# Kernel tuning notes

Measured on AMD Instinct MI355X. Metric: run time of the kernel, lower is better.

## Reference

```python
import jax, jax.numpy as jnp
import numpy as np

QMAX = 127.0          # int8 clip bound (symmetric, preserve-zero)
QDIV = 127.5          # AQT int8 scale divisor: 2**(bits-1) - 0.5


def _safe(s):
    # avoid div-by-zero for all-zero rows/cols
    return jnp.where(s == 0.0, 1.0, s)


def setup_inputs() -> dict:
    key = jax.random.key(0)
    k1, k2 = jax.random.split(key)
    lhs = jax.random.normal(k1, (8192, 4096), dtype=jnp.float32)
    rhs = jax.random.normal(k2, (4096, 4096), dtype=jnp.float32)
    return {"lhs": lhs, "rhs": rhs}


def reference(lhs, rhs):
    # --- dynamic symmetric int8 quantization (AQT abs-max calibration) ---
    # lhs: contract over axis 1 -> per-row scale [M, 1]
    s_l = _safe(jnp.max(jnp.abs(lhs), axis=1, keepdims=True) / QDIV)
    # rhs: contract over axis 0 -> per-column scale [1, N]
    s_r = _safe(jnp.max(jnp.abs(rhs), axis=0, keepdims=True) / QDIV)

    q_l = jnp.clip(jnp.round(lhs / s_l), -QMAX, QMAX).astype(jnp.int8)
    q_r = jnp.clip(jnp.round(rhs / s_r), -QMAX, QMAX).astype(jnp.int8)

    # --- integer matmul with int32 accumulation ---
    acc = jax.lax.dot_general(
        q_l, q_r,
        dimension_numbers=(((1,), (0,)), ((), ())),
        preferred_element_type=jnp.int32,
    )

    # --- dequantize: outer product of per-row / per-column scales ---
    return acc.astype(jnp.float32) * s_l * s_r
```

## Files before the change

kernel.cpp:

```cpp
#include <hip/hip_runtime.h>
#include <stdint.h>

#define M_DIM 8192
#define N_DIM 4096
#define K_DIM 4096
#define QMAXF 127.0f
#define QDIVF 127.5f

typedef int v4i __attribute__((ext_vector_type(4)));

typedef __attribute__((address_space(3))) void lds_void_t;
typedef __attribute__((address_space(1))) const void glb_void_t;

static __device__ __forceinline__ void load_lds16(const void* g, void* l) {
    __builtin_amdgcn_global_load_lds((glb_void_t*)g, (lds_void_t*)l, 16, 0, 0);
}

__global__ __launch_bounds__(256) void row_scale_kernel(
        const float* __restrict__ lhs, float* __restrict__ sL) {
    const int row = blockIdx.x;
    const float4* rp = (const float4*)(lhs + (size_t)row * K_DIM);
    const int t = threadIdx.x;
    float m = 0.0f;
#pragma unroll
    for (int i = 0; i < 4; ++i) {
        float4 v = rp[t + i * 256];
        m = fmaxf(m, fmaxf(fmaxf(fabsf(v.x), fabsf(v.y)),
                           fmaxf(fabsf(v.z), fabsf(v.w))));
    }
#pragma unroll
    for (int off = 32; off; off >>= 1) m = fmaxf(m, __shfl_down(m, off, 64));
    __shared__ float wmax[4];
    if ((t & 63) == 0) wmax[t >> 6] = m;
    __syncthreads();
    if (t == 0) {
        float mm = fmaxf(fmaxf(wmax[0], wmax[1]), fmaxf(wmax[2], wmax[3]));
        float s = mm / QDIVF;
        sL[row] = (s == 0.0f) ? 1.0f : s;
    }
}

__global__ __launch_bounds__(256) void col_absmax_kernel(
        const float* __restrict__ rhs, unsigned* __restrict__ bits) {
    const int col = blockIdx.x * 256 + threadIdx.x;
    const int r0 = blockIdx.y * 64;
    float m = 0.0f;
#pragma unroll 4
    for (int r = 0; r < 64; ++r)
        m = fmaxf(m, fabsf(rhs[(size_t)(r0 + r) * N_DIM + col]));
    atomicMax(&bits[col], __float_as_uint(m));
}

__global__ __launch_bounds__(256) void col_scale_kernel(
        const unsigned* __restrict__ bits, float* __restrict__ sR) {
    const int c = blockIdx.x * 256 + threadIdx.x;
    float s = __uint_as_float(bits[c]) / QDIVF;
    sR[c] = (s == 0.0f) ? 1.0f : s;
}

__global__ __launch_bounds__(256) void quant_lhs_kernel(
        const float* __restrict__ lhs, const float* __restrict__ sL,
        int8_t* __restrict__ ql) {
    const size_t idx = (size_t)blockIdx.x * 256 + threadIdx.x;
    const int row = (int)(idx >> 10);
    const float s = sL[row];
    float4 v = ((const float4*)lhs)[idx];
    int q0 = (int)fminf(fmaxf(rintf(v.x / s), -QMAXF), QMAXF);
    int q1 = (int)fminf(fmaxf(rintf(v.y / s), -QMAXF), QMAXF);
    int q2 = (int)fminf(fmaxf(rintf(v.z / s), -QMAXF), QMAXF);
    int q3 = (int)fminf(fmaxf(rintf(v.w / s), -QMAXF), QMAXF);
    unsigned packed = (q0 & 255) | ((q1 & 255) << 8) | ((q2 & 255) << 16)
                    | ((unsigned)(q3 & 255) << 24);
    ((unsigned*)ql)[idx] = packed;
}

__global__ __launch_bounds__(256) void quant_rhs_t_kernel(
        const float* __restrict__ rhs, const float* __restrict__ sR,
        int8_t* __restrict__ qbT) {
    __shared__ __align__(16) int8_t lt[64][80];
    const int n0 = blockIdx.x * 64;
    const int k0 = blockIdx.y * 64;
    const int t = threadIdx.x;
    const int nloc = t & 63;
    const int kq = (t >> 6) * 16;
    const float s = sR[n0 + nloc];
#pragma unroll
    for (int i = 0; i < 4; ++i) {
        unsigned pack = 0;
#pragma unroll
        for (int j = 0; j < 4; ++j) {
            int kk = kq + i * 4 + j;
            float x = rhs[(size_t)(k0 + kk) * N_DIM + n0 + nloc];
            int q = (int)fminf(fmaxf(rintf(x / s), -QMAXF), QMAXF);
            pack |= (unsigned)(q & 255) << (8 * j);
        }
        *(unsigned*)&lt[nloc][kq + i * 4] = pack;
    }
    __syncthreads();
    const int nn = t >> 2, ch = t & 3;
    v4i val = *(const v4i*)&lt[nn][ch * 16];
    *(v4i*)&qbT[(size_t)(n0 + nn) * K_DIM + k0 + ch * 16] = val;
}

__global__ __launch_bounds__(256, 2) void gemm_i8_kernel(
        const int8_t* __restrict__ qa, const int8_t* __restrict__ qbT,
        const float* __restrict__ sL, const float* __restrict__ sR,
        float* __restrict__ out) {
    __shared__ __align__(16) int8_t lds_a[128 * 64];
    __shared__ __align__(16) int8_t lds_b[128 * 64];

    const int t = threadIdx.x;
    const int wave = t >> 6;
    const int lane = t & 63;
    const int brow = blockIdx.y * 128;
    const int bcol = blockIdx.x * 128;
    const int wm = (wave >> 1) * 64;
    const int wn = (wave & 1) * 64;

    const int srow = t >> 2;
    const int pc = t & 3;
    const int cswz = pc ^ ((srow >> 1) & 3);

    int a_off[4], b_off[4];
#pragma unroll
    for (int m = 0; m < 4; ++m) {
        int row = wm + m * 16 + (lane & 15);
        int pch = (lane >> 4) ^ ((row >> 1) & 3);
        a_off[m] = row * 64 + pch * 16;
    }
#pragma unroll
    for (int n = 0; n < 4; ++n) {
        int row = wn + n * 16 + (lane & 15);
        int pch = (lane >> 4) ^ ((row >> 1) & 3);
        b_off[n] = row * 64 + pch * 16;
    }

    v4i acc[4][4];
#pragma unroll
    for (int m = 0; m < 4; ++m)
#pragma unroll
        for (int n = 0; n < 4; ++n) acc[m][n] = (v4i){0, 0, 0, 0};

    const int8_t* gA = qa  + (size_t)(brow + srow) * K_DIM + cswz * 16;
    const int8_t* gB = qbT + (size_t)(bcol + srow) * K_DIM + cswz * 16;
    const size_t pass_stride = (size_t)64 * K_DIM;

    int8_t* ldsA0 = lds_a + wave * 1024;
    int8_t* ldsA1 = lds_a + 4096 + wave * 1024;
    int8_t* ldsB0 = lds_b + wave * 1024;
    int8_t* ldsB1 = lds_b + 4096 + wave * 1024;

    for (int k0 = 0; k0 < K_DIM; k0 += 64) {
        __syncthreads();
        load_lds16(gA + k0,               ldsA0);
        load_lds16(gA + k0 + pass_stride, ldsA1);
        load_lds16(gB + k0,               ldsB0);
        load_lds16(gB + k0 + pass_stride, ldsB1);
        __syncthreads();

        v4i af[4], bf[4];
#pragma unroll
        for (int m = 0; m < 4; ++m) af[m] = *(const v4i*)(lds_a + a_off[m]);
#pragma unroll
        for (int n = 0; n < 4; ++n) bf[n] = *(const v4i*)(lds_b + b_off[n]);
#pragma unroll
        for (int m = 0; m < 4; ++m)
#pragma unroll
            for (int n = 0; n < 4; ++n)
                acc[m][n] = __builtin_amdgcn_mfma_i32_16x16x64_i8(
                        af[m], bf[n], acc[m][n], 0, 0, 0);
    }

    const int r4 = (lane >> 4) * 4;
    const int cc = lane & 15;
#pragma unroll
    for (int m = 0; m < 4; ++m) {
        const int grow0 = brow + wm + m * 16 + r4;
        const float s0 = sL[grow0 + 0];
        const float s1 = sL[grow0 + 1];
        const float s2 = sL[grow0 + 2];
        const float s3 = sL[grow0 + 3];
#pragma unroll
        for (int n = 0; n < 4; ++n) {
            const int gcol = bcol + wn + n * 16 + cc;
            const float sc = sR[gcol];
            float* o = out + (size_t)grow0 * N_DIM + gcol;
            o[0 * N_DIM] = (float)acc[m][n][0] * s0 * sc;
            o[1 * N_DIM] = (float)acc[m][n][1] * s1 * sc;
            o[2 * N_DIM] = (float)acc[m][n][2] * s2 * sc;
            o[3 * N_DIM] = (float)acc[m][n][3] * s3 * sc;
        }
    }
}

extern "C" void kernel_launch(void* const* d_in, const int* in_sizes, int n_in,
                              void* d_out, int out_size, void* d_ws, size_t ws_size,
                              hipStream_t stream) {
    const float* lhs = (const float*)d_in[0];
    const float* rhs = (const float*)d_in[1];
    float* out = (float*)d_out;

    uint8_t* ws = (uint8_t*)d_ws;
    int8_t* ql    = (int8_t*)ws;
    int8_t* qbT   = (int8_t*)(ws + 33554432);
    float* sL     = (float*)(ws + 50331648);
    float* sR     = (float*)(ws + 50331648 + 32768);
    unsigned* bits = (unsigned*)(ws + 50331648 + 32768 + 16384);

    hipMemsetAsync(bits, 0, N_DIM * sizeof(unsigned), stream);

    row_scale_kernel<<<M_DIM, 256, 0, stream>>>(lhs, sL);
    col_absmax_kernel<<<dim3(N_DIM / 256, K_DIM / 64), 256, 0, stream>>>(rhs, bits);
    col_scale_kernel<<<N_DIM / 256, 256, 0, stream>>>(bits, sR);
    quant_lhs_kernel<<<(M_DIM * K_DIM / 4) / 256, 256, 0, stream>>>(lhs, sL, ql);
    quant_rhs_t_kernel<<<dim3(N_DIM / 64, K_DIM / 64), 256, 0, stream>>>(rhs, sR, qbT);
    gemm_i8_kernel<<<dim3(N_DIM / 128, M_DIM / 128), 256, 0, stream>>>(ql, qbT, sL, sR, out);
}
```

Before: 257.1 us.

## Rewrite int8 GEMM with 256x256 tiles, double-buffered LDS pipeline and block swizzle

Replaces the 128x128, single-stage int8 GEMM with a 512-thread, 256x256-tile kernel using K=128 steps. Global-to-LDS loads for the next tile are interleaved with MFMA phases in a ping-pong buffer, using explicit vmcnt waits, barriers and s_setprio. An XOR LDS swizzle avoids bank conflicts, and the block index is remapped for L2 locality. This targets load latency and synchronisation stalls and increases data reuse. In exchange it uses 128KB of LDS, a large accumulator register footprint, and hand-tuned wait counts that are fragile.

```diff
diff --git a/kernel.cpp b/kernel.cpp
--- a/kernel.cpp
+++ b/kernel.cpp
@@ -102,79 +102,139 @@
     *(v4i*)&qbT[(size_t)(n0 + nn) * K_DIM + k0 + ch * 16] = val;
 }
 
-__global__ __launch_bounds__(256, 2) void gemm_i8_kernel(
+
+#define BAR() do { asm volatile("" ::: "memory");          \
+                   __builtin_amdgcn_s_barrier();           \
+                   asm volatile("" ::: "memory"); } while (0)
+
+#define STAGE_A(h, kt, p) do {                                                        \
+    load_lds16(gA0 + (size_t)((h) * 128) * K_DIM + (size_t)(kt) * 128,                \
+               lds + (p) * 32768 + (h) * 16384 + wb);                                 \
+    load_lds16(gA0 + (size_t)((h) * 128 + 64) * K_DIM + (size_t)(kt) * 128,           \
+               lds + (p) * 32768 + (h) * 16384 + 8192 + wb);                          \
+} while (0)
+
+#define STAGE_B(h, kt, p) do {                                                        \
+    load_lds16(gB0 + (size_t)((h) * 128) * K_DIM + (size_t)(kt) * 128,                \
+               lds + 65536 + (p) * 32768 + (h) * 16384 + wb);                         \
+    load_lds16(gB0 + (size_t)((h) * 128 + 64) * K_DIM + (size_t)(kt) * 128,           \
+               lds + 65536 + (p) * 32768 + (h) * 16384 + 8192 + wb);                  \
+} while (0)
+
+#define MFMA16(MB)                                                                    \
+    _Pragma("unroll") for (int mm = 0; mm < 4; ++mm)                                  \
+    _Pragma("unroll") for (int nn = 0; nn < 4; ++nn)                                  \
+        acc[(MB) + mm][nn] = __builtin_amdgcn_mfma_i32_16x16x64_i8(                   \
+            af[mm], bf[nn], acc[(MB) + mm][nn], 0, 0, 0);
+
+#define TILE(TT, P, S1, S2) do {                                                      \
+                                   \
+    _Pragma("unroll") for (int nn = 0; nn < 4; ++nn)                                  \
+        bf[nn] = *(const v4i*)(lds + (P) * 32768 + boff[nn * 2 + 0]);                 \
+    _Pragma("unroll") for (int mm = 0; mm < 4; ++mm)                                  \
+        af[mm] = *(const v4i*)(lds + (P) * 32768 + aoff[mm * 2 + 0]);                 \
+    if (S1) STAGE_B(1, (TT) + 1, (P) ^ 1);                                            \
+    BAR();                                                                            \
+    __builtin_amdgcn_s_setprio(1); MFMA16(0); __builtin_amdgcn_s_setprio(0);          \
+    BAR();                                                                            \
+                                   \
+    _Pragma("unroll") for (int mm = 0; mm < 4; ++mm)                                  \
+        af[mm] = *(const v4i*)(lds + (P) * 32768 + aoff[(4 + mm) * 2 + 0]);           \
+    if (S1) STAGE_A(0, (TT) + 1, (P) ^ 1);                                            \
+    BAR();                                                                            \
+    __builtin_amdgcn_s_setprio(1); MFMA16(4); __builtin_amdgcn_s_setprio(0);          \
+    BAR();                                                                            \
+                                   \
+    _Pragma("unroll") for (int nn = 0; nn < 4; ++nn)                                  \
+        bf[nn] = *(const v4i*)(lds + (P) * 32768 + boff[nn * 2 + 1]);                 \
+    _Pragma("unroll") for (int mm = 0; mm < 4; ++mm)                                  \
+        af[mm] = *(const v4i*)(lds + (P) * 32768 + aoff[mm * 2 + 1]);                 \
+    if (S1) STAGE_A(1, (TT) + 1, (P) ^ 1);                                            \
+    BAR();                                                                            \
+    __builtin_amdgcn_s_setprio(1); MFMA16(0); __builtin_amdgcn_s_setprio(0);          \
+    BAR();                                                                            \
+                    \
+    _Pragma("unroll") for (int mm = 0; mm < 4; ++mm)                                  \
+        af[mm] = *(const v4i*)(lds + (P) * 32768 + aoff[(4 + mm) * 2 + 1]);           \
+    if (S2) {                                                                         \
+        STAGE_B(0, (TT) + 2, (P));                                                    \
+        asm volatile("s_waitcnt vmcnt(2)" ::: "memory");                              \
+    } else {                                                                          \
+        asm volatile("s_waitcnt vmcnt(0)" ::: "memory");                              \
+    }                                                                                 \
+    BAR();                                                                            \
+    __builtin_amdgcn_s_setprio(1); MFMA16(4); __builtin_amdgcn_s_setprio(0);          \
+    BAR();                                                                            \
+} while (0)
+
+__global__ __launch_bounds__(512, 2) void gemm_i8_kernel(
         const int8_t* __restrict__ qa, const int8_t* __restrict__ qbT,
         const float* __restrict__ sL, const float* __restrict__ sR,
         float* __restrict__ out) {
-    __shared__ __align__(16) int8_t lds_a[128 * 64];
-    __shared__ __align__(16) int8_t lds_b[128 * 64];
+    __shared__ __align__(16) int8_t lds[131072];
 
     const int t = threadIdx.x;
     const int wave = t >> 6;
     const int lane = t & 63;
-    const int brow = blockIdx.y * 128;
-    const int bcol = blockIdx.x * 128;
-    const int wm = (wave >> 1) * 64;
-    const int wn = (wave & 1) * 64;
-
-    const int srow = t >> 2;
-    const int pc = t & 3;
-    const int cswz = pc ^ ((srow >> 1) & 3);
-
-    int a_off[4], b_off[4];
-#pragma unroll
-    for (int m = 0; m < 4; ++m) {
+
+    const int bid = blockIdx.x;
+    const int swz = (bid & 7) * 64 + (bid >> 3);
+    const int brow = (swz & 31) * 256;
+    const int bcol = (swz >> 5) * 256;
+
+    const int wm = (wave >> 2) * 128;
+    const int wn = (wave & 3) * 64;
+
+    int aoff[16];
+    int boff[8];
+#pragma unroll
+    for (int m = 0; m < 8; ++m) {
         int row = wm + m * 16 + (lane & 15);
-        int pch = (lane >> 4) ^ ((row >> 1) & 3);
-        a_off[m] = row * 64 + pch * 16;
+#pragma unroll
+        for (int ks = 0; ks < 2; ++ks)
+            aoff[m * 2 + ks] = row * 128 + ((ks * 4 + (lane >> 4)) ^ (row & 7)) * 16;
     }
 #pragma unroll
     for (int n = 0; n < 4; ++n) {
         int row = wn + n * 16 + (lane & 15);
-        int pch = (lane >> 4) ^ ((row >> 1) & 3);
-        b_off[n] = row * 64 + pch * 16;
-    }
-
-    v4i acc[4][4];
-#pragma unroll
-    for (int m = 0; m < 4; ++m)
+#pragma unroll
+        for (int ks = 0; ks < 2; ++ks)
+            boff[n * 2 + ks] = 65536 + row * 128 + ((ks * 4 + (lane >> 4)) ^ (row & 7)) * 16;
+    }
+
+    v4i acc[8][4];
+#pragma unroll
+    for (int m = 0; m < 8; ++m)
 #pragma unroll
         for (int n = 0; n < 4; ++n) acc[m][n] = (v4i){0, 0, 0, 0};
 
-    const int8_t* gA = qa  + (size_t)(brow + srow) * K_DIM + cswz * 16;
-    const int8_t* gB = qbT + (size_t)(bcol + srow) * K_DIM + cswz * 16;
-    const size_t pass_stride = (size_t)64 * K_DIM;
-
-    int8_t* ldsA0 = lds_a + wave * 1024;
-    int8_t* ldsA1 = lds_a + 4096 + wave * 1024;
-    int8_t* ldsB0 = lds_b + wave * 1024;
-    int8_t* ldsB1 = lds_b + 4096 + wave * 1024;
-
-    for (int k0 = 0; k0 < K_DIM; k0 += 64) {
-        __syncthreads();
-        load_lds16(gA + k0,               ldsA0);
-        load_lds16(gA + k0 + pass_stride, ldsA1);
-        load_lds16(gB + k0,               ldsB0);
-        load_lds16(gB + k0 + pass_stride, ldsB1);
-        __syncthreads();
-
-        v4i af[4], bf[4];
-#pragma unroll
-        for (int m = 0; m < 4; ++m) af[m] = *(const v4i*)(lds_a + a_off[m]);
-#pragma unroll
-        for (int n = 0; n < 4; ++n) bf[n] = *(const v4i*)(lds_b + b_off[n]);
-#pragma unroll
-        for (int m = 0; m < 4; ++m)
-#pragma unroll
-            for (int n = 0; n < 4; ++n)
-                acc[m][n] = __builtin_amdgcn_mfma_i32_16x16x64_i8(
-                        af[m], bf[n], acc[m][n], 0, 0, 0);
-    }
+    const int srow = t >> 3;
+    const int scol = ((t & 7) ^ (srow & 7)) * 16;
+    const int8_t* gA0 = qa  + (size_t)(brow + srow) * K_DIM + scol;
+    const int8_t* gB0 = qbT + (size_t)(bcol + srow) * K_DIM + scol;
+    const int wb = (t >> 6) * 1024;
+
+    v4i af[4], bf[4];
+
+    STAGE_B(0, 0, 0);
+    STAGE_B(1, 0, 0);
+    STAGE_A(0, 0, 0);
+    STAGE_A(1, 0, 0);
+    STAGE_B(0, 1, 1);
+    asm volatile("s_waitcnt vmcnt(2)" ::: "memory");
+    BAR();
+
+    for (int tt = 0; tt < 30; tt += 2) {
+        TILE(tt, 0, 1, 1);
+        TILE(tt + 1, 1, 1, 1);
+    }
+    TILE(30, 0, 1, 0);
+    TILE(31, 1, 0, 0);
 
     const int r4 = (lane >> 4) * 4;
     const int cc = lane & 15;
 #pragma unroll
-    for (int m = 0; m < 4; ++m) {
+    for (int m = 0; m < 8; ++m) {
         const int grow0 = brow + wm + m * 16 + r4;
         const float s0 = sL[grow0 + 0];
         const float s1 = sL[grow0 + 1];
@@ -214,5 +274,5 @@
     col_scale_kernel<<<N_DIM / 256, 256, 0, stream>>>(bits, sR);
     quant_lhs_kernel<<<(M_DIM * K_DIM / 4) / 256, 256, 0, stream>>>(lhs, sL, ql);
     quant_rhs_t_kernel<<<dim3(N_DIM / 64, K_DIM / 64), 256, 0, stream>>>(rhs, sR, qbT);
-    gemm_i8_kernel<<<dim3(N_DIM / 128, M_DIM / 128), 256, 0, stream>>>(ql, qbT, sL, sR, out);
-}
+    gemm_i8_kernel<<<dim3(M_DIM / 256 * N_DIM / 256), 512, 0, stream>>>(ql, qbT, sL, sR, out);
+}
```

Measured after the change: 231.3 us. -10.0%, faster.

## Fuse lhs scale with quantization and rewrite int8 GEMM with 256x256 multistage pipeline

Applied to the files above, without the earlier changes.

Merges the per-row absmax and lhs quantization into one kernel that keeps the row in registers, so lhs is read from memory once instead of twice. The int8 GEMM moves to 256x256 block tiles with 8 waves and a 4-buffer LDS ring filled by direct global-to-LDS loads three tiles ahead. It uses split barriers, explicit vmcnt waits, raised MFMA priority and a swizzled block order for L2 reuse. This adds register pressure and 128KB of LDS per block, which limits occupancy to one block per CU.

```diff
diff --git a/kernel.cpp b/kernel.cpp
--- a/kernel.cpp
+++ b/kernel.cpp
@@ -16,27 +16,38 @@
     __builtin_amdgcn_global_load_lds((glb_void_t*)g, (lds_void_t*)l, 16, 0, 0);
 }
 
-__global__ __launch_bounds__(256) void row_scale_kernel(
-        const float* __restrict__ lhs, float* __restrict__ sL) {
+__global__ __launch_bounds__(256) void row_quant_kernel(
+        const float* __restrict__ lhs, float* __restrict__ sL,
+        int8_t* __restrict__ ql) {
     const int row = blockIdx.x;
     const float4* rp = (const float4*)(lhs + (size_t)row * K_DIM);
     const int t = threadIdx.x;
+    float4 v[4];
     float m = 0.0f;
 #pragma unroll
     for (int i = 0; i < 4; ++i) {
-        float4 v = rp[t + i * 256];
-        m = fmaxf(m, fmaxf(fmaxf(fabsf(v.x), fabsf(v.y)),
-                           fmaxf(fabsf(v.z), fabsf(v.w))));
+        v[i] = rp[t + i * 256];
+        m = fmaxf(m, fmaxf(fmaxf(fabsf(v[i].x), fabsf(v[i].y)),
+                           fmaxf(fabsf(v[i].z), fabsf(v[i].w))));
     }
 #pragma unroll
     for (int off = 32; off; off >>= 1) m = fmaxf(m, __shfl_down(m, off, 64));
     __shared__ float wmax[4];
     if ((t & 63) == 0) wmax[t >> 6] = m;
     __syncthreads();
-    if (t == 0) {
-        float mm = fmaxf(fmaxf(wmax[0], wmax[1]), fmaxf(wmax[2], wmax[3]));
-        float s = mm / QDIVF;
-        sL[row] = (s == 0.0f) ? 1.0f : s;
+    const float mm = fmaxf(fmaxf(wmax[0], wmax[1]), fmaxf(wmax[2], wmax[3]));
+    float s = mm / QDIVF;
+    s = (s == 0.0f) ? 1.0f : s;
+    if (t == 0) sL[row] = s;
+    unsigned* qo = (unsigned*)ql + (size_t)row * 1024;
+#pragma unroll
+    for (int i = 0; i < 4; ++i) {
+        int q0 = (int)fminf(fmaxf(rintf(v[i].x / s), -QMAXF), QMAXF);
+        int q1 = (int)fminf(fmaxf(rintf(v[i].y / s), -QMAXF), QMAXF);
+        int q2 = (int)fminf(fmaxf(rintf(v[i].z / s), -QMAXF), QMAXF);
+        int q3 = (int)fminf(fmaxf(rintf(v[i].w / s), -QMAXF), QMAXF);
+        qo[t + i * 256] = (q0 & 255) | ((q1 & 255) << 8) | ((q2 & 255) << 16)
+                        | ((unsigned)(q3 & 255) << 24);
     }
 }
 
@@ -56,22 +67,6 @@
     const int c = blockIdx.x * 256 + threadIdx.x;
     float s = __uint_as_float(bits[c]) / QDIVF;
     sR[c] = (s == 0.0f) ? 1.0f : s;
-}
-
-__global__ __launch_bounds__(256) void quant_lhs_kernel(
-        const float* __restrict__ lhs, const float* __restrict__ sL,
-        int8_t* __restrict__ ql) {
-    const size_t idx = (size_t)blockIdx.x * 256 + threadIdx.x;
-    const int row = (int)(idx >> 10);
-    const float s = sL[row];
-    float4 v = ((const float4*)lhs)[idx];
-    int q0 = (int)fminf(fmaxf(rintf(v.x / s), -QMAXF), QMAXF);
-    int q1 = (int)fminf(fmaxf(rintf(v.y / s), -QMAXF), QMAXF);
-    int q2 = (int)fminf(fmaxf(rintf(v.z / s), -QMAXF), QMAXF);
-    int q3 = (int)fminf(fmaxf(rintf(v.w / s), -QMAXF), QMAXF);
-    unsigned packed = (q0 & 255) | ((q1 & 255) << 8) | ((q2 & 255) << 16)
-                    | ((unsigned)(q3 & 255) << 24);
-    ((unsigned*)ql)[idx] = packed;
 }
 
 __global__ __launch_bounds__(256) void quant_rhs_t_kernel(
@@ -102,74 +97,108 @@
     *(v4i*)&qbT[(size_t)(n0 + nn) * K_DIM + k0 + ch * 16] = val;
 }
 
-__global__ __launch_bounds__(256, 2) void gemm_i8_kernel(
+
+#define BAR() do { asm volatile("" ::: "memory");          \
+                   __builtin_amdgcn_s_barrier();           \
+                   asm volatile("" ::: "memory"); } while (0)
+
+#define VMCNT(N) asm volatile("s_waitcnt vmcnt(%0)" :: "n"(N) : "memory")
+
+#define STAGE_A(h, kt, bq) \
+    load_lds16(gA0 + (size_t)((h) * 128) * K_DIM + (size_t)(kt) * 64, \
+               lds + (bq) * 16384 + (h) * 8192 + sdst)
+#define STAGE_B(h, kt, bq) \
+    load_lds16(gB0 + (size_t)((h) * 128) * K_DIM + (size_t)(kt) * 64, \
+               lds + 65536 + (bq) * 16384 + (h) * 8192 + sdst)
+
+#define MFMA16(NB)                                                              \
+    _Pragma("unroll") for (int mm = 0; mm < 4; ++mm)                            \
+    _Pragma("unroll") for (int nn = 0; nn < 4; ++nn)                            \
+        acc[mm][(NB) + nn] = __builtin_amdgcn_mfma_i32_16x16x64_i8(             \
+            af[mm], bf[nn], acc[mm][(NB) + nn], 0, 0, 0);
+
+#define TILE(KT, BUF, S, VM) do {                                               \
+                        \
+    _Pragma("unroll") for (int mm = 0; mm < 4; ++mm)                            \
+        af[mm] = *(const v4i*)(lds + (BUF) * 16384 + aoff[mm]);                 \
+    _Pragma("unroll") for (int nn = 0; nn < 4; ++nn)                            \
+        bf[nn] = *(const v4i*)(lds + (BUF) * 16384 + boff[nn]);                 \
+    if (S) { STAGE_A(0, (KT) + 3, ((BUF) + 3) & 3);                             \
+             STAGE_A(1, (KT) + 3, ((BUF) + 3) & 3); }                           \
+    BAR();                                                                      \
+    __builtin_amdgcn_s_setprio(1); MFMA16(0); __builtin_amdgcn_s_setprio(0);    \
+    BAR();                                                                      \
+                 \
+    _Pragma("unroll") for (int nn = 0; nn < 4; ++nn)                            \
+        bf[nn] = *(const v4i*)(lds + (BUF) * 16384 + boff[4 + nn]);             \
+    if (S) { STAGE_B(0, (KT) + 3, ((BUF) + 3) & 3);                             \
+             STAGE_B(1, (KT) + 3, ((BUF) + 3) & 3); }                           \
+    VMCNT(VM);                                                                  \
+    BAR();                                                                      \
+    __builtin_amdgcn_s_setprio(1); MFMA16(4); __builtin_amdgcn_s_setprio(0);    \
+    BAR();                                                                      \
+} while (0)
+
+__global__ __launch_bounds__(512, 2) void gemm_i8_kernel(
         const int8_t* __restrict__ qa, const int8_t* __restrict__ qbT,
         const float* __restrict__ sL, const float* __restrict__ sR,
         float* __restrict__ out) {
-    __shared__ __align__(16) int8_t lds_a[128 * 64];
-    __shared__ __align__(16) int8_t lds_b[128 * 64];
+    __shared__ __align__(16) int8_t lds[131072];
 
     const int t = threadIdx.x;
     const int wave = t >> 6;
     const int lane = t & 63;
-    const int brow = blockIdx.y * 128;
-    const int bcol = blockIdx.x * 128;
+
+    const int bid = blockIdx.x;
+    const int swz = (bid & 7) * 64 + (bid >> 3);
+    const int brow = (swz & 31) * 256;
+    const int bcol = (swz >> 5) * 256;
+
     const int wm = (wave >> 1) * 64;
-    const int wn = (wave & 1) * 64;
-
-    const int srow = t >> 2;
-    const int pc = t & 3;
-    const int cswz = pc ^ ((srow >> 1) & 3);
-
-    int a_off[4], b_off[4];
+    const int wn = (wave & 1) * 128;
+
+    int aoff[4], boff[8];
 #pragma unroll
     for (int m = 0; m < 4; ++m) {
         int row = wm + m * 16 + (lane & 15);
-        int pch = (lane >> 4) ^ ((row >> 1) & 3);
-        a_off[m] = row * 64 + pch * 16;
-    }
-#pragma unroll
-    for (int n = 0; n < 4; ++n) {
+        aoff[m] = row * 64 + (((lane >> 4) ^ ((row >> 1) & 3)) * 16);
+    }
+#pragma unroll
+    for (int n = 0; n < 8; ++n) {
         int row = wn + n * 16 + (lane & 15);
-        int pch = (lane >> 4) ^ ((row >> 1) & 3);
-        b_off[n] = row * 64 + pch * 16;
-    }
-
-    v4i acc[4][4];
+        boff[n] = 65536 + row * 64 + (((lane >> 4) ^ ((row >> 1) & 3)) * 16);
+    }
+
+    v4i acc[4][8];
 #pragma unroll
     for (int m = 0; m < 4; ++m)
 #pragma unroll
-        for (int n = 0; n < 4; ++n) acc[m][n] = (v4i){0, 0, 0, 0};
-
-    const int8_t* gA = qa  + (size_t)(brow + srow) * K_DIM + cswz * 16;
-    const int8_t* gB = qbT + (size_t)(bcol + srow) * K_DIM + cswz * 16;
-    const size_t pass_stride = (size_t)64 * K_DIM;
-
-    int8_t* ldsA0 = lds_a + wave * 1024;
-    int8_t* ldsA1 = lds_a + 4096 + wave * 1024;
-    int8_t* ldsB0 = lds_b + wave * 1024;
-    int8_t* ldsB1 = lds_b + 4096 + wave * 1024;
-
-    for (int k0 = 0; k0 < K_DIM; k0 += 64) {
-        __syncthreads();
-        load_lds16(gA + k0,               ldsA0);
-        load_lds16(gA + k0 + pass_stride, ldsA1);
-        load_lds16(gB + k0,               ldsB0);
-        load_lds16(gB + k0 + pass_stride, ldsB1);
-        __syncthreads();
-
-        v4i af[4], bf[4];
-#pragma unroll
-        for (int m = 0; m < 4; ++m) af[m] = *(const v4i*)(lds_a + a_off[m]);
-#pragma unroll
-        for (int n = 0; n < 4; ++n) bf[n] = *(const v4i*)(lds_b + b_off[n]);
-#pragma unroll
-        for (int m = 0; m < 4; ++m)
-#pragma unroll
-            for (int n = 0; n < 4; ++n)
-                acc[m][n] = __builtin_amdgcn_mfma_i32_16x16x64_i8(
-                        af[m], bf[n], acc[m][n], 0, 0, 0);
-    }
+        for (int n = 0; n < 8; ++n) acc[m][n] = (v4i){0, 0, 0, 0};
+
+    const int srow = t >> 2;
+    const int lc = (t & 3) ^ ((srow >> 1) & 3);
+    const int8_t* gA0 = qa  + (size_t)(brow + srow) * K_DIM + lc * 16;
+    const int8_t* gB0 = qbT + (size_t)(bcol + srow) * K_DIM + lc * 16;
+    const int sdst = t * 16;
+
+    v4i af[4], bf[4];
+
+    STAGE_A(0, 0, 0); STAGE_A(1, 0, 0); STAGE_B(0, 0, 0); STAGE_B(1, 0, 0);
+    STAGE_A(0, 1, 1); STAGE_A(1, 1, 1); STAGE_B(0, 1, 1); STAGE_B(1, 1, 1);
+    STAGE_A(0, 2, 2); STAGE_A(1, 2, 2); STAGE_B(0, 2, 2); STAGE_B(1, 2, 2);
+    VMCNT(8);
+    BAR();
+
+    for (int kt = 0; kt < 60; kt += 4) {
+        TILE(kt + 0, 0, 1, 8);
+        TILE(kt + 1, 1, 1, 8);
+        TILE(kt + 2, 2, 1, 8);
+        TILE(kt + 3, 3, 1, 8);
+    }
+    TILE(60, 0, 1, 8);
+    TILE(61, 1, 0, 4);
+    TILE(62, 2, 0, 0);
+    TILE(63, 3, 0, 0);
 
     const int r4 = (lane >> 4) * 4;
     const int cc = lane & 15;
@@ -181,7 +210,7 @@
         const float s2 = sL[grow0 + 2];
         const float s3 = sL[grow0 + 3];
 #pragma unroll
-        for (int n = 0; n < 4; ++n) {
+        for (int n = 0; n < 8; ++n) {
             const int gcol = bcol + wn + n * 16 + cc;
             const float sc = sR[gcol];
             float* o = out + (size_t)grow0 * N_DIM + gcol;
@@ -209,10 +238,9 @@
 
     hipMemsetAsync(bits, 0, N_DIM * sizeof(unsigned), stream);
 
-    row_scale_kernel<<<M_DIM, 256, 0, stream>>>(lhs, sL);
+    row_quant_kernel<<<M_DIM, 256, 0, stream>>>(lhs, sL, ql);
     col_absmax_kernel<<<dim3(N_DIM / 256, K_DIM / 64), 256, 0, stream>>>(rhs, bits);
     col_scale_kernel<<<N_DIM / 256, 256, 0, stream>>>(bits, sR);
-    quant_lhs_kernel<<<(M_DIM * K_DIM / 4) / 256, 256, 0, stream>>>(lhs, sL, ql);
     quant_rhs_t_kernel<<<dim3(N_DIM / 64, K_DIM / 64), 256, 0, stream>>>(rhs, sR, qbT);
-    gemm_i8_kernel<<<dim3(N_DIM / 128, M_DIM / 128), 256, 0, stream>>>(ql, qbT, sL, sR, out);
-}
+    gemm_i8_kernel<<<dim3(M_DIM / 256 * N_DIM / 256), 512, 0, stream>>>(ql, qbT, sL, sR, out);
+}
```

Result: faster. 223.6 us (-13.0%).
